# Optimization experiments

Hardware: AMD Instinct MI355X
Metric: run time of the kernel (lower is better)

The kernel has to match this reference:

```python
import jax, jax.numpy as jnp
import numpy as np

INPUT_SIZE = 128
HIDDEN_SIZE = 128
BATCH = 65536


def _xavier(key, shape):
    fan_out, fan_in = shape
    limit = np.sqrt(6.0 / (fan_in + fan_out)).astype(np.float32)
    return jax.random.uniform(key, shape, jnp.float32, -limit, limit)


def setup_inputs() -> dict:
    key = jax.random.key(0)
    ks = jax.random.split(key, 12)
    inp = {
        "x": jax.random.normal(ks[0], (BATCH, INPUT_SIZE), jnp.float32),
        "h_t": jax.random.normal(ks[1], (BATCH, HIDDEN_SIZE), jnp.float32),
        "c_t": jax.random.normal(ks[2], (BATCH, HIDDEN_SIZE), jnp.float32),
        "W_ii": _xavier(ks[3], (HIDDEN_SIZE, INPUT_SIZE)),
        "W_hi": _xavier(ks[4], (HIDDEN_SIZE, HIDDEN_SIZE)),
        "b_i": jnp.zeros((HIDDEN_SIZE,), jnp.float32),
        "W_if": _xavier(ks[5], (HIDDEN_SIZE, INPUT_SIZE)),
        "W_hf": _xavier(ks[6], (HIDDEN_SIZE, HIDDEN_SIZE)),
        "b_f": jnp.zeros((HIDDEN_SIZE,), jnp.float32),
        "W_ig": _xavier(ks[7], (HIDDEN_SIZE, INPUT_SIZE)),
        "W_hg": _xavier(ks[8], (HIDDEN_SIZE, HIDDEN_SIZE)),
        "b_g": jnp.zeros((HIDDEN_SIZE,), jnp.float32),
        "W_io": _xavier(ks[9], (HIDDEN_SIZE, INPUT_SIZE)),
        "W_ho": _xavier(ks[10], (HIDDEN_SIZE, HIDDEN_SIZE)),
        "b_o": jnp.zeros((HIDDEN_SIZE,), jnp.float32),
    }
    return inp


def reference(x, h_t, c_t, W_ii, W_hi, b_i, W_if, W_hf, b_f, W_ig, W_hg, b_g, W_io, W_ho, b_o):
    # Fuse the 8 small GEMMs into 2 concatenated GEMMs, identical math to
    # per-gate F.linear calls (same weights, just stacked along output dim).
    W_x = jnp.concatenate([W_ii, W_if, W_ig, W_io], axis=0)   # [4H, I]
    W_h = jnp.concatenate([W_hi, W_hf, W_hg, W_ho], axis=0)   # [4H, H]
    b = jnp.concatenate([b_i, b_f, b_g, b_o], axis=0)         # [4H]
    gates = x @ W_x.T + h_t @ W_h.T + b                       # [B, 4H]
    i_a, f_a, g_a, o_a = jnp.split(gates, 4, axis=1)
    i_t = jax.nn.sigmoid(i_a)
    f_t = jax.nn.sigmoid(f_a)
    g_t = jnp.tanh(g_a)
    o_t = jax.nn.sigmoid(o_a)
    c_new = f_t * c_t + i_t * g_t
    h_new = o_t * jnp.tanh(c_new)
    return (h_new, c_new)
```

## Files before the change

kernel.cpp:

```cpp
#include <hip/hip_runtime.h>
#include <hip/hip_bf16.h>


typedef short s16x8 __attribute__((ext_vector_type(8)));
typedef float f32x4 __attribute__((ext_vector_type(4)));

__device__ __forceinline__ short f2bf(float f) {
    __hip_bfloat16 h = __float2bfloat16(f);
    return __builtin_bit_cast(short, h);
}
__device__ __forceinline__ float sigm(float x) { return 1.0f / (1.0f + __expf(-x)); }
__device__ __forceinline__ float tanh_f(float x) { return 1.0f - 2.0f / (1.0f + __expf(2.0f * x)); }

__global__ __launch_bounds__(256)
void repack_weights(const float* __restrict__ Wii, const float* __restrict__ Whi,
                    const float* __restrict__ Wif, const float* __restrict__ Whf,
                    const float* __restrict__ Wig, const float* __restrict__ Whg,
                    const float* __restrict__ Wio, const float* __restrict__ Who,
                    short* __restrict__ ws)
{
    const int t   = blockIdx.x * 256 + threadIdx.x;
    const int fi  = t >> 6;
    const int l   = t & 63;
    const int ks  = fi & 7;
    const int g   = (fi >> 3) & 3;
    const int jt  = fi >> 5;
    const int j   = jt * 16 + (l & 15);
    const int k   = ks * 32 + (l >> 4) * 8;

    const float* wx = (g == 0) ? Wii : (g == 1) ? Wif : (g == 2) ? Wig : Wio;
    const float* wh = (g == 0) ? Whi : (g == 1) ? Whf : (g == 2) ? Whg : Who;
    const float* src = (k < 128) ? (wx + (size_t)j * 128 + k)
                                 : (wh + (size_t)j * 128 + (k - 128));
    f32x4 a = *(const f32x4*)src;
    f32x4 b = *(const f32x4*)(src + 4);
    s16x8 v;
#pragma unroll
    for (int q = 0; q < 4; ++q) { v[q] = f2bf(a[q]); v[4 + q] = f2bf(b[q]); }
    *(s16x8*)(ws + (size_t)t * 8) = v;
}

__global__ __launch_bounds__(512, 4)
void lstm_cell_kernel(const float* __restrict__ X,
                      const float* __restrict__ H,
                      const float* __restrict__ C,
                      const float* __restrict__ Bi, const float* __restrict__ Bf,
                      const float* __restrict__ Bg, const float* __restrict__ Bo,
                      const short* __restrict__ WS,
                      float* __restrict__ OutH,
                      float* __restrict__ OutC)
{
    __shared__ __align__(16) char sA[16384];

    const int tid = threadIdx.x;
    const int l   = tid & 63;
    const int w   = tid >> 6;
    const int lj  = l & 15;
    const int lq  = l >> 4;
    const int jw  = w * 16 + lj;
    const int B0  = blockIdx.x * 32;

    const float* abase = (w < 4) ? X : H;
    const int    colr  = (w & 3) * 32 + lq * 8;
    f32x4 sa[2], sb[2];
#pragma unroll
    for (int mt = 0; mt < 2; ++mt) {
        const float* p = abase + (size_t)(B0 + mt * 16 + lj) * 128 + colr;
        sa[mt] = *(const f32x4*)p;
        sb[mt] = *(const f32x4*)(p + 4);
    }

    const short* wsw = WS + (size_t)(w * 4) * 8 * 512 + (size_t)l * 8;
    s16x8 wbuf[2][4];
#pragma unroll
    for (int g = 0; g < 4; ++g) {
        wbuf[0][g] = *(const s16x8*)(wsw + (size_t)(g * 8 + 0) * 512);
        wbuf[1][g] = *(const s16x8*)(wsw + (size_t)(g * 8 + 1) * 512);
    }

    float cpv[8];
#pragma unroll
    for (int mt = 0; mt < 2; ++mt)
#pragma unroll
        for (int r = 0; r < 4; ++r)
            cpv[mt * 4 + r] = C[(size_t)(B0 + mt * 16 + lq * 4 + r) * 128 + jw];

    const float bi  = Bi[jw];
    const float bfv = Bf[jw];
    const float bg  = Bg[jw];
    const float bo  = Bo[jw];

#pragma unroll
    for (int mt = 0; mt < 2; ++mt) {
        s16x8 v;
#pragma unroll
        for (int q = 0; q < 4; ++q) {
            v[q]     = f2bf(sa[mt][q]);
            v[4 + q] = f2bf(sb[mt][q]);
        }
        *(s16x8*)(sA + (mt * 8 + w) * 1024 + l * 16) = v;
    }
    asm volatile("s_waitcnt lgkmcnt(0)\n\ts_barrier" ::: "memory");

    f32x4 acc[2][4];
#pragma unroll
    for (int mt = 0; mt < 2; ++mt)
#pragma unroll
        for (int g = 0; g < 4; ++g)
            acc[mt][g] = (f32x4){0.f, 0.f, 0.f, 0.f};

#pragma unroll
    for (int ks = 0; ks < 8; ++ks) {
        const s16x8 af0 = *(const s16x8*)(sA + (0 * 8 + ks) * 1024 + l * 16);
        const s16x8 af1 = *(const s16x8*)(sA + (1 * 8 + ks) * 1024 + l * 16);
#pragma unroll
        for (int g = 0; g < 4; ++g) {
            acc[0][g] = __builtin_amdgcn_mfma_f32_16x16x32_bf16(af0, wbuf[ks & 1][g], acc[0][g], 0, 0, 0);
            acc[1][g] = __builtin_amdgcn_mfma_f32_16x16x32_bf16(af1, wbuf[ks & 1][g], acc[1][g], 0, 0, 0);
        }
        if (ks < 6) {
#pragma unroll
            for (int g = 0; g < 4; ++g)
                wbuf[ks & 1][g] = *(const s16x8*)(wsw + (size_t)(g * 8 + ks + 2) * 512);
        }
    }

#pragma unroll
    for (int mt = 0; mt < 2; ++mt) {
#pragma unroll
        for (int r = 0; r < 4; ++r) {
            const int b = B0 + mt * 16 + lq * 4 + r;
            const size_t idx = (size_t)b * 128 + jw;
            const float ia = acc[mt][0][r] + bi;
            const float fa = acc[mt][1][r] + bfv;
            const float ga = acc[mt][2][r] + bg;
            const float oa = acc[mt][3][r] + bo;
            const float it = sigm(ia);
            const float ft = sigm(fa);
            const float gt = tanh_f(ga);
            const float ot = sigm(oa);
            const float co = cpv[mt * 4 + r];
            const float cn = ft * co + it * gt;
            const float hn = ot * tanh_f(cn);
            OutH[idx] = hn;
            OutC[idx] = cn;
        }
    }
}

extern "C" void kernel_launch(void* const* d_in, const int* in_sizes, int n_in,
                              void* d_out, int out_size, void* d_ws, size_t ws_size,
                              hipStream_t stream) {
    const float* X   = (const float*)d_in[0];
    const float* H   = (const float*)d_in[1];
    const float* C   = (const float*)d_in[2];
    const float* Wii = (const float*)d_in[3];
    const float* Whi = (const float*)d_in[4];
    const float* Bi  = (const float*)d_in[5];
    const float* Wif = (const float*)d_in[6];
    const float* Whf = (const float*)d_in[7];
    const float* Bf  = (const float*)d_in[8];
    const float* Wig = (const float*)d_in[9];
    const float* Whg = (const float*)d_in[10];
    const float* Bg  = (const float*)d_in[11];
    const float* Wio = (const float*)d_in[12];
    const float* Who = (const float*)d_in[13];
    const float* Bo  = (const float*)d_in[14];

    short* ws = (short*)d_ws;

    hipLaunchKernelGGL(repack_weights, dim3(64), dim3(256), 0, stream,
                       Wii, Whi, Wif, Whf, Wig, Whg, Wio, Who, ws);

    float* OutH = (float*)d_out;
    float* OutC = OutH + (size_t)65536 * 128;

    hipLaunchKernelGGL(lstm_cell_kernel, dim3(2048), dim3(512), 0, stream,
                       X, H, C, Bi, Bf, Bg, Bo, ws, OutH, OutC);
}
```

Before: 193.8 us.

## Split each 32-row block across two 256-thread blocks by hidden-column half

Each block now covers half of the hidden columns (4 of 8 16-column tiles) for 32 batch rows, using 256 threads, and the grid doubles to 4096 blocks. Every block still stages the full 32x256 bf16 activation tile into shared memory, so each wave loads two activation slices. X and H are therefore read twice across the pair of blocks. The weight prefetch pipeline deepens from 2 to 4 k-steps, and the launch bounds change to 256 threads with 3 blocks per SM. The aim is finer-grained scheduling and more load-latency hiding, at the cost of duplicated input reads and higher register pressure.

```diff
diff --git a/kernel.cpp b/kernel.cpp
--- a/kernel.cpp
+++ b/kernel.cpp
@@ -40,7 +40,7 @@
     *(s16x8*)(ws + (size_t)t * 8) = v;
 }
 
-__global__ __launch_bounds__(512, 4)
+__global__ __launch_bounds__(256, 3)
 void lstm_cell_kernel(const float* __restrict__ X,
                       const float* __restrict__ H,
                       const float* __restrict__ C,
@@ -57,26 +57,31 @@
     const int w   = tid >> 6;
     const int lj  = l & 15;
     const int lq  = l >> 4;
-    const int jw  = w * 16 + lj;
-    const int B0  = blockIdx.x * 32;
+    const int qb  = blockIdx.x & 1;
+    const int B0  = (blockIdx.x >> 1) * 32;
+    const int jt16 = qb * 4 + w;
+    const int jw   = jt16 * 16 + lj;
 
-    const float* abase = (w < 4) ? X : H;
-    const int    colr  = (w & 3) * 32 + lq * 8;
-    f32x4 sa[2], sb[2];
+    const float* abase = (w < 2) ? X : H;
+    f32x4 sa[2][2], sb[2][2];
 #pragma unroll
-    for (int mt = 0; mt < 2; ++mt) {
-        const float* p = abase + (size_t)(B0 + mt * 16 + lj) * 128 + colr;
-        sa[mt] = *(const f32x4*)p;
-        sb[mt] = *(const f32x4*)(p + 4);
+    for (int s = 0; s < 2; ++s) {
+        const int kloc = (((2 * w + s) & 3) * 32) + lq * 8;
+#pragma unroll
+        for (int mt = 0; mt < 2; ++mt) {
+            const float* p = abase + (size_t)(B0 + mt * 16 + lj) * 128 + kloc;
+            sa[s][mt] = *(const f32x4*)p;
+            sb[s][mt] = *(const f32x4*)(p + 4);
+        }
     }
 
-    const short* wsw = WS + (size_t)(w * 4) * 8 * 512 + (size_t)l * 8;
-    s16x8 wbuf[2][4];
+    const short* wsw = WS + (size_t)jt16 * 32 * 512 + (size_t)l * 8;
+    s16x8 wbuf[4][4];
 #pragma unroll
-    for (int g = 0; g < 4; ++g) {
-        wbuf[0][g] = *(const s16x8*)(wsw + (size_t)(g * 8 + 0) * 512);
-        wbuf[1][g] = *(const s16x8*)(wsw + (size_t)(g * 8 + 1) * 512);
-    }
+    for (int d = 0; d < 4; ++d)
+#pragma unroll
+        for (int g = 0; g < 4; ++g)
+            wbuf[d][g] = *(const s16x8*)(wsw + (size_t)(g * 8 + d) * 512);
 
     float cpv[8];
 #pragma unroll
@@ -91,15 +96,17 @@
     const float bo  = Bo[jw];
 
 #pragma unroll
-    for (int mt = 0; mt < 2; ++mt) {
-        s16x8 v;
+    for (int s = 0; s < 2; ++s)
 #pragma unroll
-        for (int q = 0; q < 4; ++q) {
-            v[q]     = f2bf(sa[mt][q]);
-            v[4 + q] = f2bf(sb[mt][q]);
+        for (int mt = 0; mt < 2; ++mt) {
+            s16x8 v;
+#pragma unroll
+            for (int q = 0; q < 4; ++q) {
+                v[q]     = f2bf(sa[s][mt][q]);
+                v[4 + q] = f2bf(sb[s][mt][q]);
+            }
+            *(s16x8*)(sA + (mt * 8 + 2 * w + s) * 1024 + l * 16) = v;
         }
-        *(s16x8*)(sA + (mt * 8 + w) * 1024 + l * 16) = v;
-    }
     asm volatile("s_waitcnt lgkmcnt(0)\n\ts_barrier" ::: "memory");
 
     f32x4 acc[2][4];
@@ -115,13 +122,13 @@
         const s16x8 af1 = *(const s16x8*)(sA + (1 * 8 + ks) * 1024 + l * 16);
 #pragma unroll
         for (int g = 0; g < 4; ++g) {
-            acc[0][g] = __builtin_amdgcn_mfma_f32_16x16x32_bf16(af0, wbuf[ks & 1][g], acc[0][g], 0, 0, 0);
-            acc[1][g] = __builtin_amdgcn_mfma_f32_16x16x32_bf16(af1, wbuf[ks & 1][g], acc[1][g], 0, 0, 0);
+            acc[0][g] = __builtin_amdgcn_mfma_f32_16x16x32_bf16(af0, wbuf[ks & 3][g], acc[0][g], 0, 0, 0);
+            acc[1][g] = __builtin_amdgcn_mfma_f32_16x16x32_bf16(af1, wbuf[ks & 3][g], acc[1][g], 0, 0, 0);
         }
-        if (ks < 6) {
+        if (ks < 4) {
 #pragma unroll
             for (int g = 0; g < 4; ++g)
-                wbuf[ks & 1][g] = *(const s16x8*)(wsw + (size_t)(g * 8 + ks + 2) * 512);
+                wbuf[ks & 3][g] = *(const s16x8*)(wsw + (size_t)(g * 8 + ks + 4) * 512);
         }
     }
 
@@ -175,6 +182,6 @@
     float* OutH = (float*)d_out;
     float* OutC = OutH + (size_t)65536 * 128;
 
-    hipLaunchKernelGGL(lstm_cell_kernel, dim3(2048), dim3(512), 0, stream,
+    hipLaunchKernelGGL(lstm_cell_kernel, dim3(4096), dim3(256), 0, stream,
                        X, H, C, Bi, Bf, Bg, Bo, ws, OutH, OutC);
 }
```

Measured after the change: 201.6 us. +4.0%, slower.
